# Kernel tuning notes

Measured on AMD Instinct MI355X. Metric: run time of the kernel, lower is better.

## Reference

```python
import jax, jax.numpy as jnp
import numpy as np

H = 8          # attention heads
D = 16         # per-head dim (hidden // heads)
HID = 128      # hidden_channels
OUT = 8        # out_channels of final linear
L = 2          # num_layers
NP = 100000    # num paper nodes
NA = 100000    # num author nodes
E = 500000     # edges per edge type
NEG_SLOPE = 0.2


def setup_inputs() -> dict:
    key = jax.random.key(0)
    ks = jax.random.split(key, 20)
    def nrm(k, shape, s=0.05):
        return jax.random.normal(k, shape, dtype=jnp.float32) * s
    return {
        'x_paper': jax.random.normal(ks[0], (NP, HID), dtype=jnp.float32),
        'x_author': jax.random.normal(ks[1], (NA, HID), dtype=jnp.float32),
        'Wp_p': nrm(ks[2], (L, HID, HID)),
        'bp_p': jnp.zeros((L, HID), jnp.float32),
        'Wp_a': nrm(ks[3], (L, HID, HID)),
        'bp_a': jnp.zeros((L, HID), jnp.float32),
        'as_ap': nrm(ks[4], (L, H, D), 0.2),
        'ad_ap': nrm(ks[5], (L, H, D), 0.2),
        'as_pa': nrm(ks[6], (L, H, D), 0.2),
        'ad_pa': nrm(ks[7], (L, H, D), 0.2),
        'as_pp': nrm(ks[8], (L, H, D), 0.2),
        'ad_pp': nrm(ks[9], (L, H, D), 0.2),
        'Wk': nrm(ks[10], (L, HID, HID)),
        'bk': jnp.zeros((L, HID), jnp.float32),
        'q': nrm(ks[11], (L, HID), 0.2),
        'Wout': nrm(ks[12], (HID, OUT)),
        'bout': jnp.zeros((OUT,), jnp.float32),
        'ei_ap': jax.random.randint(ks[13], (2, E), 0, NP, dtype=jnp.int32),
        'ei_pa': jax.random.randint(ks[14], (2, E), 0, NP, dtype=jnp.int32),
        'ei_pp': jax.random.randint(ks[15], (2, E), 0, NP, dtype=jnp.int32),
    }


def _leaky_relu(x):
    return jnp.where(x >= 0, x, NEG_SLOPE * x)


def _seg_softmax(alpha, dst, n):
    # PyG-style segment softmax over incoming edges of each dst node
    amax = jax.ops.segment_max(alpha, dst, num_segments=n)
    a = jnp.exp(alpha - amax[dst])
    denom = jax.ops.segment_sum(a, dst, num_segments=n) + 1e-16
    return a / denom[dst]


def _edge_attn_agg(z_src, z_dst, ei, a_s, a_d, n_dst):
    # per-edge-type GAT-style attention + scatter aggregate (HANConv message/aggregate)
    src, dst = ei[0], ei[1]
    alpha_src = (z_src * a_s).sum(-1)   # [Ns, H]
    alpha_dst = (z_dst * a_d).sum(-1)   # [Nd, H]
    alpha = _leaky_relu(alpha_src[src] + alpha_dst[dst])  # [E, H]
    alpha = _seg_softmax(alpha, dst, n_dst)
    msg = z_src[src] * alpha[:, :, None]                   # [E, H, D]
    out = jax.ops.segment_sum(msg, dst, num_segments=n_dst)
    return jax.nn.relu(out.reshape(n_dst, H * D))


def _group(outs, q, Wk, bk):
    # HANConv semantic-level attention across metapaths
    stacked = jnp.stack(outs)                               # [K, N, F]
    score = (q * jnp.tanh(stacked @ Wk + bk).mean(1)).sum(-1)  # [K]
    attn = jax.nn.softmax(score)
    return (attn[:, None, None] * stacked).sum(0)           # [N, F]


def _han_conv(xp, xa, ei_ap, ei_pa, ei_pp, Wp_p, bp_p, Wp_a, bp_a,
              as_ap, ad_ap, as_pa, ad_pa, as_pp, ad_pp, Wk, bk, q):
    zp = (xp @ Wp_p + bp_p).reshape(-1, H, D)
    za = (xa @ Wp_a + bp_a).reshape(-1, H, D)
    n_p, n_a = zp.shape[0], za.shape[0]
    out_ap = _edge_attn_agg(za, zp, ei_ap, as_ap, ad_ap, n_p)  # author -> paper
    out_pa = _edge_attn_agg(zp, za, ei_pa, as_pa, ad_pa, n_a)  # paper -> author
    out_pp = _edge_attn_agg(zp, zp, ei_pp, as_pp, ad_pp, n_p)  # paper -> paper
    new_xp = _group([out_ap, out_pp], q, Wk, bk)
    new_xa = _group([out_pa], q, Wk, bk)
    return new_xp, new_xa


def _forward(x_paper, x_author, Wp_p, bp_p, Wp_a, bp_a, as_ap, ad_ap,
             as_pa, ad_pa, as_pp, ad_pp, Wk, bk, q, Wout, bout,
             ei_ap, ei_pa, ei_pp):
    xp, xa = x_paper, x_author
    for l in range(L):
        xp, xa = _han_conv(xp, xa, ei_ap, ei_pa, ei_pp,
                           Wp_p[l], bp_p[l], Wp_a[l], bp_a[l],
                           as_ap[l], ad_ap[l], as_pa[l], ad_pa[l],
                           as_pp[l], ad_pp[l], Wk[l], bk[l], q[l])
        if l < L - 1:
            xp = jax.nn.elu(xp)  # dropout identity in eval mode (p applied only in training)
            xa = jax.nn.elu(xa)
    tgt = jax.nn.elu(xp)
    return tgt @ Wout + bout  # [NP, OUT]


def reference(x_paper, x_author, Wp_p, bp_p, Wp_a, bp_a, as_ap, ad_ap,
              as_pa, ad_pa, as_pp, ad_pp, Wk, bk, q, Wout, bout,
              ei_ap, ei_pa, ei_pp):
    return _forward(x_paper, x_author, Wp_p, bp_p, Wp_a, bp_a, as_ap, ad_ap,
                    as_pa, ad_pa, as_pp, ad_pp, Wk, bk, q, Wout, bout,
                    ei_ap, ei_pa, ei_pp)
```

## Files before the change

kernel.cpp:

```cpp
#include <hip/hip_runtime.h>

#define NHID 128
#define NHEAD 8
#define NNODE 100000
#define NEDGE 500000
#define NEG 0.2f
#define SCORE_GRID 512
#define GEMM_GRID 512
#define AGG_BLOCKS 12500
#define EB ((NEDGE + 255) / 256)
#define SB ((NNODE + 1023) / 1024)

typedef float4 f4;
typedef __attribute__((ext_vector_type(8))) short bfrag;
typedef __attribute__((ext_vector_type(4))) float facc;

__device__ inline float b2f(unsigned int u) {
    return __uint_as_float(u << 16);
}
__device__ inline unsigned short f2b(float f) {
    unsigned int u = __float_as_uint(f);
    unsigned int r = (u + 0x7FFFu + ((u >> 16) & 1u)) >> 16;
    return (unsigned short)r;
}
__device__ inline float fast_tanh(float x) {
    float e = __expf(2.f * x);
    return 1.f - 2.f / (e + 1.f);
}

struct WavSet {
    const float* W; const float* b;
    const float* v0; const float* v1; const float* v2; const float* v3;
    ushort* GT; float* bAv;
};

__global__ __launch_bounds__(256) void prep_fused(
    const float* __restrict__ w0, const float* __restrict__ w1,
    const float* __restrict__ w2, const float* __restrict__ w3,
    const float* __restrict__ w4, const float* __restrict__ w5,
    ushort* __restrict__ o0, ushort* __restrict__ o1,
    ushort* __restrict__ o2, ushort* __restrict__ o3,
    ushort* __restrict__ o4, ushort* __restrict__ o5,
    WavSet s0, WavSet s1, WavSet s2, WavSet s3,
    const int* __restrict__ e0, const int* __restrict__ e1,
    const int* __restrict__ e2, int* __restrict__ deg3)
{
    const int b = blockIdx.x;
    if (b < 384) {
        int which = b >> 6;
        int i = (b & 63) * 256 + threadIdx.x;
        const float* W = (which == 0) ? w0 : (which == 1) ? w1 : (which == 2) ? w2
                       : (which == 3) ? w3 : (which == 4) ? w4 : w5;
        ushort* Wt = (which == 0) ? o0 : (which == 1) ? o1 : (which == 2) ? o2
                   : (which == 3) ? o3 : (which == 4) ? o4 : o5;
        int fi = i >> 3, e = i & 7;
        int jk = fi >> 6, l = fi & 63;
        int j = jk >> 2, kk = jk & 3;
        int lr = l & 15, lg = l >> 4;
        Wt[i] = f2b(W[(kk * 32 + lg * 8 + e) * 128 + j * 16 + lr]);
    } else if (b < 448) {
        int bb = b - 384;
        int which = bb >> 4;
        const WavSet s = (which == 0) ? s0 : (which == 1) ? s1 : (which == 2) ? s2 : s3;
        int i = (bb & 15) * 256 + threadIdx.x;
        int fi = i >> 3, e = i & 7;
        int jk = fi >> 6, l = fi & 63;
        int jt = jk >> 2, kk = jk & 3;
        int lr = l & 15, lg = l >> 4;
        int c = jt * 16 + lr;
        int m = kk * 32 + lg * 8 + e;
        int vec = c >> 3, h = c & 7;
        const float* vp = (vec == 0) ? s.v0 : (vec == 1) ? s.v1 : (vec == 2) ? s.v2 : s.v3;
        float sv = 0.f;
        if (vp) {
            #pragma unroll
            for (int dd = 0; dd < 16; ++dd)
                sv = fmaf(s.W[m * 128 + h * 16 + dd], vp[h * 16 + dd], sv);
        }
        s.GT[i] = f2b(sv);
        if (i < 32) {
            int cc = i, vv = cc >> 3, hh = cc & 7;
            const float* vq = (vv == 0) ? s.v0 : (vv == 1) ? s.v1 : (vv == 2) ? s.v2 : s.v3;
            float t = 0.f;
            if (vq) {
                #pragma unroll
                for (int dd = 0; dd < 16; ++dd)
                    t = fmaf(s.b[hh * 16 + dd], vq[hh * 16 + dd], t);
            }
            s.bAv[cc] = t;
        }
    } else {
        int bb2 = b - 448;
        int ty = bb2 / EB, bb = bb2 % EB;
        const int* ei = (ty == 0) ? e0 : (ty == 1) ? e1 : e2;
        int e = bb * 256 + threadIdx.x;
        if (e < NEDGE) atomicAdd(deg3 + ty * NNODE + ei[NEDGE + e], 1);
    }
}

struct PArgs {
    const void* A;
    const ushort* A2;
    const ushort* WtT;
    const ushort* GT;
    const float* bias;
    const float* bAv;
    ushort* C;
    float* ao0; float* ao1; float* ao2; float* ao3;
    int mode;
};

template<int M0, int M1, int SCAT>
__global__ __launch_bounds__(256) void gemm_persist(
    PArgs g0, PArgs g1, const float* __restrict__ attn, int nt, int N,
    const int* __restrict__ e0, const int* __restrict__ e1,
    const int* __restrict__ e2, int* __restrict__ cur3, int* __restrict__ cols3)
{
    if (SCAT && blockIdx.x >= GEMM_GRID) {
        int bb2 = blockIdx.x - GEMM_GRID;
        int ty = bb2 / EB, bb = bb2 % EB;
        const int* ei = (ty == 0) ? e0 : (ty == 1) ? e1 : e2;
        int e = bb * 256 + threadIdx.x;
        if (e < NEDGE) {
            int d = ei[NEDGE + e];
            int pos = atomicAdd(cur3 + ty * NNODE + d, 1);
            cols3[ty * NEDGE + pos] = ei[e];
        }
        return;
    }

    __shared__ uint4 smem[2560];
    const int hg = GEMM_GRID >> 1;
    const int half = (blockIdx.x >= hg) ? 1 : 0;
    const PArgs ga = half ? g1 : g0;
    const int MODE = half ? M1 : M0;
    const int b0 = half ? blockIdx.x - hg : blockIdx.x;

    const int tid = threadIdx.x;
    const int l = tid & 63, w = tid >> 6;
    const int lr = l & 15, lg = l >> 4;

    {
        const uint4* ws = reinterpret_cast<const uint4*>(ga.WtT);
        const uint4* gs = reinterpret_cast<const uint4*>(ga.GT);
        #pragma unroll
        for (int i = 0; i < 8; ++i) smem[tid + i * 256] = ws[tid + i * 256];
        #pragma unroll
        for (int i = 0; i < 2; ++i) smem[2048 + tid + i * 256] = gs[tid + i * 256];
    }
    float a0 = 0.f, a1 = 0.f;
    if (MODE == 2) { a0 = attn[0]; a1 = attn[1]; }
    __syncthreads();
    const ushort* WtL = reinterpret_cast<const ushort*>(smem);
    const ushort* GL  = WtL + 16384;

    float bv[8];
    #pragma unroll
    for (int j = 0; j < 8; ++j) bv[j] = ga.bias[j * 16 + lr];
    float bA[2];
    #pragma unroll
    for (int jt = 0; jt < 2; ++jt) bA[jt] = ga.bAv[jt * 16 + lr];

    uint4 rawA[(M0 == 0 && M1 == 0) ? 8 : 16];

    auto load_raw = [&](int t) {
        const int rw0 = t * 128 + w * 32;
        #pragma unroll
        for (int i = 0; i < 2; ++i) {
            int r = rw0 + i * 16 + lr; r = (r < N) ? r : (N - 1);
            if (MODE == 1) {
                const float* ap = (const float*)ga.A + (size_t)r * 128 + lg * 8;
                #pragma unroll
                for (int kk = 0; kk < 4; ++kk) {
                    rawA[i * 8 + kk * 2]     = *reinterpret_cast<const uint4*>(ap + kk * 32);
                    rawA[i * 8 + kk * 2 + 1] = *reinterpret_cast<const uint4*>(ap + kk * 32 + 4);
                }
            } else {
                const ushort* ap = (const ushort*)ga.A + (size_t)r * 128 + lg * 8;
                #pragma unroll
                for (int kk = 0; kk < 4; ++kk)
                    rawA[i * 4 + kk] = *reinterpret_cast<const uint4*>(ap + kk * 32);
                if (MODE == 2) {
                    const ushort* ap2 = ga.A2 + (size_t)r * 128 + lg * 8;
                    #pragma unroll
                    for (int kk = 0; kk < 4; ++kk)
                        rawA[8 + i * 4 + kk] = *reinterpret_cast<const uint4*>(ap2 + kk * 32);
                }
            }
        }
    };

    if (b0 >= nt) return;
    load_raw(b0);

    for (int t = b0; t < nt; t += hg) {
        const int rw0 = t * 128 + w * 32;

        bfrag av_[2][4];
        #pragma unroll
        for (int i = 0; i < 2; ++i) {
            #pragma unroll
            for (int kk = 0; kk < 4; ++kk) {
                if (MODE == 0) {
                    av_[i][kk] = *reinterpret_cast<bfrag*>(&rawA[i * 4 + kk]);
                } else if (MODE == 1) {
                    uint4 u = rawA[i * 8 + kk * 2];
                    uint4 v = rawA[i * 8 + kk * 2 + 1];
                    bfrag fr;
                    fr[0] = (short)f2b(__uint_as_float(u.x));
                    fr[1] = (short)f2b(__uint_as_float(u.y));
                    fr[2] = (short)f2b(__uint_as_float(u.z));
                    fr[3] = (short)f2b(__uint_as_float(u.w));
                    fr[4] = (short)f2b(__uint_as_float(v.x));
                    fr[5] = (short)f2b(__uint_as_float(v.y));
                    fr[6] = (short)f2b(__uint_as_float(v.z));
                    fr[7] = (short)f2b(__uint_as_float(v.w));
                    av_[i][kk] = fr;
                } else {
                    uint4 ua = rawA[i * 4 + kk];
                    uint4 ub = rawA[8 + i * 4 + kk];
                    unsigned int aa[4] = {ua.x, ua.y, ua.z, ua.w};
                    unsigned int bb[4] = {ub.x, ub.y, ub.z, ub.w};
                    bfrag fr;
                    #pragma unroll
                    for (int q = 0; q < 4; ++q) {
                        float lo = a0 * b2f(aa[q] & 0xffffu) + a1 * b2f(bb[q] & 0xffffu);
                        float hi = a0 * b2f(aa[q] >> 16)     + a1 * b2f(bb[q] >> 16);
                        fr[q * 2]     = (short)f2b(lo);
                        fr[q * 2 + 1] = (short)f2b(hi);
                    }
                    av_[i][kk] = fr;
                }
            }
        }

        if (t + hg < nt) load_raw(t + hg);

        facc accC[2][8], accP[2][2];
        #pragma unroll
        for (int i = 0; i < 2; ++i) {
            #pragma unroll
            for (int j = 0; j < 8; ++j) accC[i][j] = (facc){0.f, 0.f, 0.f, 0.f};
            #pragma unroll
            for (int jt = 0; jt < 2; ++jt) accP[i][jt] = (facc){0.f, 0.f, 0.f, 0.f};
        }

        #pragma unroll
        for (int kk = 0; kk < 4; ++kk) {
            #pragma unroll
            for (int j = 0; j < 8; ++j) {
                bfrag bfr = *reinterpret_cast<const bfrag*>(WtL + ((j * 4 + kk) * 64 + l) * 8);
                #pragma unroll
                for (int i = 0; i < 2; ++i)
                    accC[i][j] = __builtin_amdgcn_mfma_f32_16x16x32_bf16(
                        av_[i][kk], bfr, accC[i][j], 0, 0, 0);
            }
            #pragma unroll
            for (int jt = 0; jt < 2; ++jt) {
                bfrag gfr = *reinterpret_cast<const bfrag*>(GL + ((jt * 4 + kk) * 64 + l) * 8);
                #pragma unroll
                for (int i = 0; i < 2; ++i)
                    accP[i][jt] = __builtin_amdgcn_mfma_f32_16x16x32_bf16(
                        av_[i][kk], gfr, accP[i][jt], 0, 0, 0);
            }
        }

        #pragma unroll
        for (int j = 0; j < 8; ++j) {
            #pragma unroll
            for (int i = 0; i < 2; ++i) {
                #pragma unroll
                for (int rr = 0; rr < 4; ++rr) {
                    int row = rw0 + i * 16 + lg * 4 + rr;
                    if (row < N)
                        ga.C[(size_t)row * 128 + j * 16 + lr] = f2b(accC[i][j][rr] + bv[j]);
                }
            }
        }

        #pragma unroll
        for (int jt = 0; jt < 2; ++jt) {
            int c = jt * 16 + lr;
            int vec = c >> 3, h = c & 7;
            float* ao = (vec == 0) ? ga.ao0 : (vec == 1) ? ga.ao1
                      : (vec == 2) ? ga.ao2 : ga.ao3;
            if (ao == nullptr) continue;
            #pragma unroll
            for (int i = 0; i < 2; ++i) {
                #pragma unroll
                for (int rr = 0; rr < 4; ++rr) {
                    int row = rw0 + i * 16 + lg * 4 + rr;
                    if (row < N) ao[row * 8 + h] = accP[i][jt][rr] + bA[jt];
                }
            }
        }
    }
}

__global__ __launch_bounds__(256) void score_persist(
    const ushort* __restrict__ A0, const ushort* __restrict__ A1,
    const ushort* __restrict__ WtT, const float* __restrict__ bias,
    float* __restrict__ part, int nt, int N)
{
    __shared__ uint4 smem[2048];
    __shared__ float sred[4][256];
    const int tid = threadIdx.x;
    const int l = tid & 63, w = tid >> 6;
    const int lr = l & 15, lg = l >> 4;

    {
        const uint4* ws = reinterpret_cast<const uint4*>(WtT);
        #pragma unroll
        for (int i = 0; i < 8; ++i) smem[tid + i * 256] = ws[tid + i * 256];
    }
    __syncthreads();
    const ushort* WtL = reinterpret_cast<const ushort*>(smem);

    float bv[8];
    #pragma unroll
    for (int j = 0; j < 8; ++j) bv[j] = bias[j * 16 + lr];

    float cs[2][8];
    #pragma unroll
    for (int h = 0; h < 2; ++h)
        #pragma unroll
        for (int j = 0; j < 8; ++j) cs[h][j] = 0.f;

    const int total = 2 * nt;
    for (int t = blockIdx.x; t < total; t += gridDim.x) {
        const int half = (t >= nt) ? 1 : 0;
        const ushort* A = half ? A1 : A0;
        const int bb = half ? t - nt : t;
        const int rw0 = bb * 128 + w * 32;

        bfrag av_[2][4];
        #pragma unroll
        for (int i = 0; i < 2; ++i) {
            int r = rw0 + i * 16 + lr; r = (r < N) ? r : (N - 1);
            const ushort* ap = A + (size_t)r * 128 + lg * 8;
            #pragma unroll
            for (int kk = 0; kk < 4; ++kk)
                av_[i][kk] = *reinterpret_cast<const bfrag*>(ap + kk * 32);
        }

        facc acc[2][8];
        #pragma unroll
        for (int i = 0; i < 2; ++i)
            #pragma unroll
            for (int j = 0; j < 8; ++j) acc[i][j] = (facc){0.f, 0.f, 0.f, 0.f};

        #pragma unroll
        for (int kk = 0; kk < 4; ++kk) {
            #pragma unroll
            for (int j = 0; j < 8; ++j) {
                bfrag bfr = *reinterpret_cast<const bfrag*>(WtL + ((j * 4 + kk) * 64 + l) * 8);
                #pragma unroll
                for (int i = 0; i < 2; ++i)
                    acc[i][j] = __builtin_amdgcn_mfma_f32_16x16x32_bf16(
                        av_[i][kk], bfr, acc[i][j], 0, 0, 0);
            }
        }

        #pragma unroll
        for (int j = 0; j < 8; ++j) {
            float s = 0.f;
            #pragma unroll
            for (int i = 0; i < 2; ++i) {
                #pragma unroll
                for (int r = 0; r < 4; ++r) {
                    int row = rw0 + i * 16 + lg * 4 + r;
                    if (row < N) s += fast_tanh(acc[i][j][r] + bv[j]);
                }
            }
            cs[half][j] += s;
        }
    }

    #pragma unroll
    for (int h = 0; h < 2; ++h)
        #pragma unroll
        for (int j = 0; j < 8; ++j) {
            float s = cs[h][j];
            s += __shfl_xor(s, 16, 64);
            s += __shfl_xor(s, 32, 64);
            if (lg == 0) sred[w][h * 128 + j * 16 + lr] = s;
        }
    __syncthreads();
    float tot = sred[0][tid] + sred[1][tid] + sred[2][tid] + sred[3][tid];
    part[(size_t)blockIdx.x * 256 + tid] = tot;
}

__global__ void attn_reduce(const float* __restrict__ part,
                            const float* __restrict__ qv,
                            float* __restrict__ attn, int nb)
{
    __shared__ float sm[256];
    int t = threadIdx.x;
    float s0 = 0.f, s1 = 0.f, s2 = 0.f, s3 = 0.f;
    for (int b = 0; b < nb; b += 4) {
        s0 += part[(size_t)b * 256 + t];
        s1 += part[(size_t)(b + 1) * 256 + t];
        s2 += part[(size_t)(b + 2) * 256 + t];
        s3 += part[(size_t)(b + 3) * 256 + t];
    }
    sm[t] = (s0 + s1 + s2 + s3) * qv[t & 127];
    __syncthreads();
    if (t == 0) {
        float a = 0.f, b = 0.f;
        for (int i = 0; i < 128; ++i) { a += sm[i]; b += sm[128 + i]; }
        a *= (1.0f / 100000.0f);
        b *= (1.0f / 100000.0f);
        float m = fmaxf(a, b);
        float ea = expf(a - m), eb = expf(b - m);
        float inv = 1.f / (ea + eb);
        attn[0] = ea * inv;
        attn[1] = eb * inv;
    }
}

__global__ __launch_bounds__(1024) void scan_block3(
    const int* __restrict__ deg3, int* __restrict__ offs3, int* __restrict__ bsum3)
{
    __shared__ int sd[1024];
    int ty = blockIdx.x / SB, bb = blockIdx.x % SB;
    const int* deg = deg3 + ty * NNODE;
    int* offs = offs3 + ty * (NNODE + 1);
    int t = threadIdx.x, i = bb * 1024 + t;
    int v = (i < NNODE) ? deg[i] : 0;
    sd[t] = v; __syncthreads();
    for (int o = 1; o < 1024; o <<= 1) {
        int x = (t >= o) ? sd[t - o] : 0;
        __syncthreads();
        sd[t] += x;
        __syncthreads();
    }
    if (i < NNODE) offs[i + 1] = sd[t];
    if (t == 1023) bsum3[ty * 128 + bb] = sd[t];
}

__global__ void scan_bsum3(const int* __restrict__ bsum3, int* __restrict__ boff3)
{
    int t = threadIdx.x;
    if (t < 3) {
        int run = 0;
        for (int b = 0; b < SB; ++b) { boff3[t * 128 + b] = run; run += bsum3[t * 128 + b]; }
    }
}

__global__ __launch_bounds__(1024) void scan_add3(
    int* __restrict__ offs3, const int* __restrict__ boff3, int* __restrict__ cur3)
{
    int ty = blockIdx.x / SB, bb = blockIdx.x % SB;
    int* offs = offs3 + ty * (NNODE + 1);
    int* cur = cur3 + ty * NNODE;
    int i = bb * 1024 + threadIdx.x;
    if (i == 0) { offs[0] = 0; cur[0] = 0; }
    if (i < NNODE) {
        int v = offs[i + 1] + boff3[ty * 128 + bb];
        offs[i + 1] = v;
        if (i + 1 < NNODE) cur[i + 1] = v;
    }
}

struct AggJob {
    const int* offs; const int* cols;
    const float* asrc; const float* adst;
    const ushort* z; ushort* out;
};

__global__ __launch_bounds__(256) void agg_multi(AggJob j0, AggJob j1, AggJob j2)
{
    int jb = blockIdx.x / AGG_BLOCKS;
    const AggJob jj = (jb == 0) ? j0 : (jb == 1) ? j1 : j2;
    int bb = blockIdx.x - jb * AGG_BLOCKS;
    int w = threadIdx.x >> 6;
    int lane = threadIdx.x & 63;
    int halfid = lane >> 5;
    int sl = lane & 31;
    int d = bb * 8 + w * 2 + halfid;
    int h = sl >> 2;
    float ad = jj.adst[d * 8 + h];
    int e0 = jj.offs[d], e1 = jj.offs[d + 1];
    float acc0 = 0.f, acc1 = 0.f, acc2 = 0.f, acc3 = 0.f, psum = 0.f;
    const ushort* zbase = jj.z + sl * 4;
    for (int base = e0; base < e1; base += 4) {
        int idx[4];
        #pragma unroll
        for (int i = 0; i < 4; ++i) {
            int ee = base + i;
            idx[i] = jj.cols[(ee < e1) ? ee : (e1 - 1)];
        }
        float xs[4];
        #pragma unroll
        for (int i = 0; i < 4; ++i) xs[i] = jj.asrc[idx[i] * 8 + h];
        uint2 zv[4];
        #pragma unroll
        for (int i = 0; i < 4; ++i)
            zv[i] = *reinterpret_cast<const uint2*>(zbase + (size_t)idx[i] * 128);
        #pragma unroll
        for (int i = 0; i < 4; ++i) {
            float a = xs[i] + ad;
            a = fmaxf(a, NEG * a);
            float p = __expf(a);
            p = (base + i < e1) ? p : 0.f;
            acc0 = fmaf(p, b2f(zv[i].x & 0xffffu), acc0);
            acc1 = fmaf(p, b2f(zv[i].x >> 16),     acc1);
            acc2 = fmaf(p, b2f(zv[i].y & 0xffffu), acc2);
            acc3 = fmaf(p, b2f(zv[i].y >> 16),     acc3);
            psum += p;
        }
    }
    float inv = 1.f / (psum + 1e-16f);
    uint2 pk;
    pk.x = (unsigned int)f2b(fmaxf(acc0 * inv, 0.f))
         | ((unsigned int)f2b(fmaxf(acc1 * inv, 0.f)) << 16);
    pk.y = (unsigned int)f2b(fmaxf(acc2 * inv, 0.f))
         | ((unsigned int)f2b(fmaxf(acc3 * inv, 0.f)) << 16);
    *reinterpret_cast<uint2*>(jj.out + (size_t)d * 128 + sl * 4) = pk;
}

__global__ __launch_bounds__(256) void final_gemm_mix(
    const ushort* __restrict__ XA_, const ushort* __restrict__ XB_,
    const float* __restrict__ attn, const float* __restrict__ W,
    const float* __restrict__ bias, float* __restrict__ out, int N)
{
    __shared__ float Ws[128][8];
    __shared__ __align__(16) float Xs[32][129];
    int tid = threadIdx.x;
    float a0 = attn[0], a1 = attn[1];
    for (int i = tid; i < 1024; i += 256) Ws[i >> 3][i & 7] = W[i];
    int row0 = blockIdx.x * 32;
    for (int i = tid; i < 512; i += 256) {
        int r = i >> 4, q = i & 15;
        int gr = row0 + r;
        uint4 va = make_uint4(0, 0, 0, 0), vb = make_uint4(0, 0, 0, 0);
        if (gr < N) {
            va = reinterpret_cast<const uint4*>(XA_ + (size_t)gr * 128)[q];
            vb = reinterpret_cast<const uint4*>(XB_ + (size_t)gr * 128)[q];
        }
        int c = q * 8;
        unsigned int ua[4] = {va.x, va.y, va.z, va.w};
        unsigned int ub[4] = {vb.x, vb.y, vb.z, vb.w};
        #pragma unroll
        for (int qq = 0; qq < 4; ++qq) {
            Xs[r][c + qq * 2]     = a0 * b2f(ua[qq] & 0xffffu) + a1 * b2f(ub[qq] & 0xffffu);
            Xs[r][c + qq * 2 + 1] = a0 * b2f(ua[qq] >> 16)     + a1 * b2f(ub[qq] >> 16);
        }
    }
    __syncthreads();
    int r = tid >> 3, o = tid & 7;
    int gr = row0 + r;
    if (gr < N) {
        float s = bias[o];
        #pragma unroll
        for (int k = 0; k < 128; ++k) s = fmaf(Xs[r][k], Ws[k][o], s);
        out[(size_t)gr * 8 + o] = s;
    }
}

extern "C" void kernel_launch(void* const* d_in, const int* in_sizes, int n_in,
                              void* d_out, int out_size, void* d_ws, size_t ws_size,
                              hipStream_t stream) {
    const float* x_paper  = (const float*)d_in[0];
    const float* x_author = (const float*)d_in[1];
    const float* Wp_p = (const float*)d_in[2];
    const float* bp_p = (const float*)d_in[3];
    const float* Wp_a = (const float*)d_in[4];
    const float* bp_a = (const float*)d_in[5];
    const float* as_ap = (const float*)d_in[6];
    const float* ad_ap = (const float*)d_in[7];
    const float* as_pa = (const float*)d_in[8];
    const float* ad_pa = (const float*)d_in[9];
    const float* as_pp = (const float*)d_in[10];
    const float* ad_pp = (const float*)d_in[11];
    const float* Wk   = (const float*)d_in[12];
    const float* bk   = (const float*)d_in[13];
    const float* qv   = (const float*)d_in[14];
    const float* Wout = (const float*)d_in[15];
    const float* bout = (const float*)d_in[16];
    const int* ei_ap = (const int*)d_in[17];
    const int* ei_pa = (const int*)d_in[18];
    const int* ei_pp = (const int*)d_in[19];

    const size_t NB = (size_t)NNODE * 128;
    ushort* Z0 = (ushort*)d_ws;
    ushort* Z1 = Z0 + NB;
    ushort* Z2 = Z1 + NB;
    ushort* Z3 = Z2 + NB;
    ushort* P0 = Z3 + NB;
    ushort* P1 = P0 + NB;
    float* fp = (float*)(P1 + NB);
    float* ap_s = fp; fp += NNODE * 8;
    float* ap_d = fp; fp += NNODE * 8;
    float* pa_s = fp; fp += NNODE * 8;
    float* pa_d = fp; fp += NNODE * 8;
    float* pp_s = fp; fp += NNODE * 8;
    float* pp_d = fp; fp += NNODE * 8;
    float* part = fp; fp += (size_t)SCORE_GRID * 256;
    float* attn = fp; fp += 16;
    float* bAv_p0 = fp; fp += 32;
    float* bAv_a0 = fp; fp += 32;
    float* bAv_p1 = fp; fp += 32;
    float* bAv_a1 = fp; fp += 32;
    ushort* up = (ushort*)fp;
    ushort* WtP0 = up; up += 16384;
    ushort* WtA0 = up; up += 16384;
    ushort* WtP1 = up; up += 16384;
    ushort* WtA1 = up; up += 16384;
    ushort* WtK0 = up; up += 16384;
    ushort* WtK1 = up; up += 16384;
    ushort* G_p0 = up; up += 4096;
    ushort* G_a0 = up; up += 4096;
    ushort* G_p1 = up; up += 4096;
    ushort* G_a1 = up; up += 4096;
    int* ip = (int*)(((size_t)up + 15) & ~(size_t)15);
    int* cols3 = ip; ip += 3 * NEDGE;
    int* offs3 = ip; ip += 3 * (NNODE + 1);
    int* deg3  = ip; ip += 3 * NNODE;
    int* cur3  = ip; ip += 3 * NNODE;
    int* bsum3 = ip; ip += 3 * 128;
    int* boff3 = ip; ip += 3 * 128;

    const int* cols_ap = cols3;
    const int* cols_pa = cols3 + NEDGE;
    const int* cols_pp = cols3 + 2 * NEDGE;
    const int* offs_ap = offs3;
    const int* offs_pa = offs3 + (NNODE + 1);
    const int* offs_pp = offs3 + 2 * (NNODE + 1);

    const dim3 blk(256);
    const int nt128 = (NNODE + 127) / 128;
    const int wo = 128 * 128, bo = 128, ao = 128;

    hipMemsetAsync(deg3, 0, 3 * NNODE * 4, stream);
    {
        WavSet s0{Wp_p, bp_p, ad_ap, as_pa, as_pp, ad_pp, G_p0, bAv_p0};
        WavSet s1{Wp_a, bp_a, as_ap, ad_pa, nullptr, nullptr, G_a0, bAv_a0};
        WavSet s2{Wp_p + wo, bp_p + bo, ad_ap + ao, as_pp + ao, ad_pp + ao, nullptr, G_p1, bAv_p1};
        WavSet s3{Wp_a + wo, bp_a + bo, as_ap + ao, nullptr, nullptr, nullptr, G_a1, bAv_a1};
        prep_fused<<<448 + 3 * EB, blk, 0, stream>>>(
            Wp_p, Wp_a, Wp_p + wo, Wp_a + wo, Wk, Wk + wo,
            WtP0, WtA0, WtP1, WtA1, WtK0, WtK1,
            s0, s1, s2, s3, ei_ap, ei_pa, ei_pp, deg3);
    }
    scan_block3<<<3 * SB, 1024, 0, stream>>>(deg3, offs3, bsum3);
    scan_bsum3<<<1, 64, 0, stream>>>(bsum3, boff3);
    scan_add3<<<3 * SB, 1024, 0, stream>>>(offs3, boff3, cur3);

    {
        PArgs gp{x_paper,  nullptr, WtP0, G_p0, bp_p, bAv_p0, Z0, ap_d, pa_s, pp_s, pp_d, 1};
        PArgs ga{x_author, nullptr, WtA0, G_a0, bp_a, bAv_a0, Z1, ap_s, pa_d, nullptr, nullptr, 1};
        gemm_persist<1, 1, 1><<<GEMM_GRID + 3 * EB, blk, 0, stream>>>(
            gp, ga, attn, nt128, NNODE, ei_ap, ei_pa, ei_pp, cur3, cols3);
    }

    {
        AggJob a0{offs_ap, cols_ap, ap_s, ap_d, Z1, Z2};
        AggJob a1{offs_pa, cols_pa, pa_s, pa_d, Z0, Z3};
        AggJob a2{offs_pp, cols_pp, pp_s, pp_d, Z0, P0};
        agg_multi<<<3 * AGG_BLOCKS, blk, 0, stream>>>(a0, a1, a2);
    }

    score_persist<<<SCORE_GRID, blk, 0, stream>>>(Z2, P0, WtK0, bk, part, nt128, NNODE);
    attn_reduce<<<1, 256, 0, stream>>>(part, qv, attn, SCORE_GRID);

    {
        PArgs gp{Z2, P0, WtP1, G_p1, bp_p + bo, bAv_p1, Z0, ap_d, pp_s, pp_d, nullptr, 2};
        PArgs ga{Z3, nullptr, WtA1, G_a1, bp_a + bo, bAv_a1, Z1, ap_s, nullptr, nullptr, nullptr, 0};
        gemm_persist<2, 0, 0><<<GEMM_GRID, blk, 0, stream>>>(
            gp, ga, attn, nt128, NNODE, nullptr, nullptr, nullptr, nullptr, nullptr);
    }

    {
        AggJob a0{offs_ap, cols_ap, ap_s, ap_d, Z1, Z2};
        AggJob a1{offs_pp, cols_pp, pp_s, pp_d, Z0, P1};
        agg_multi<<<2 * AGG_BLOCKS, blk, 0, stream>>>(a0, a1, a1);
    }

    score_persist<<<SCORE_GRID, blk, 0, stream>>>(Z2, P1, WtK1, bk + bo, part, nt128, NNODE);
    attn_reduce<<<1, 256, 0, stream>>>(part, qv + bo, attn, SCORE_GRID);

    final_gemm_mix<<<(NNODE + 31) / 32, blk, 0, stream>>>(Z2, P1, attn, Wout, bout, (float*)d_out, NNODE);
}
```

Baseline: 532.4 us.

## Fuse PA aggregation into score kernel, merge scan kernels, trim GEMM register staging

The paper-to-author aggregation now runs as extra blocks inside the layer-0 score kernel, so it overlaps the score GEMM and one launch disappears. The separate block-sum scan kernel is removed; each scan_add3 block sums the earlier block totals serially in one thread. The persistent GEMM keeps only one raw staging buffer: the second row group (fp32 mode) and the A2 operand (mix mode) are loaded inside the loop rather than prefetched, which lowers register pressure but exposes that load latency. The CSR column scatter uses nontemporal stores.

Result: slower. 625.8 us (+17.5%).

```diff
diff --git a/kernel.cpp b/kernel.cpp
--- a/kernel.cpp
+++ b/kernel.cpp
@@ -124,7 +124,7 @@
         if (e < NEDGE) {
             int d = ei[NEDGE + e];
             int pos = atomicAdd(cur3 + ty * NNODE + d, 1);
-            cols3[ty * NEDGE + pos] = ei[e];
+            __builtin_nontemporal_store(ei[e], cols3 + (size_t)ty * NEDGE + pos);
         }
         return;
     }
@@ -161,31 +161,28 @@
     #pragma unroll
     for (int jt = 0; jt < 2; ++jt) bA[jt] = ga.bAv[jt * 16 + lr];
 
-    uint4 rawA[(M0 == 0 && M1 == 0) ? 8 : 16];
+    uint4 rawA[8];
+
+    auto clampr = [&](int row) { return (row < N) ? row : (N - 1); };
 
     auto load_raw = [&](int t) {
         const int rw0 = t * 128 + w * 32;
-        #pragma unroll
-        for (int i = 0; i < 2; ++i) {
-            int r = rw0 + i * 16 + lr; r = (r < N) ? r : (N - 1);
-            if (MODE == 1) {
-                const float* ap = (const float*)ga.A + (size_t)r * 128 + lg * 8;
-                #pragma unroll
-                for (int kk = 0; kk < 4; ++kk) {
-                    rawA[i * 8 + kk * 2]     = *reinterpret_cast<const uint4*>(ap + kk * 32);
-                    rawA[i * 8 + kk * 2 + 1] = *reinterpret_cast<const uint4*>(ap + kk * 32 + 4);
-                }
-            } else {
+        if (MODE == 1) {
+            int r = clampr(rw0 + lr);
+            const float* ap = (const float*)ga.A + (size_t)r * 128 + lg * 8;
+            #pragma unroll
+            for (int kk = 0; kk < 4; ++kk) {
+                rawA[kk * 2]     = *reinterpret_cast<const uint4*>(ap + kk * 32);
+                rawA[kk * 2 + 1] = *reinterpret_cast<const uint4*>(ap + kk * 32 + 4);
+            }
+        } else {
+            #pragma unroll
+            for (int i = 0; i < 2; ++i) {
+                int r = clampr(rw0 + i * 16 + lr);
                 const ushort* ap = (const ushort*)ga.A + (size_t)r * 128 + lg * 8;
                 #pragma unroll
                 for (int kk = 0; kk < 4; ++kk)
                     rawA[i * 4 + kk] = *reinterpret_cast<const uint4*>(ap + kk * 32);
-                if (MODE == 2) {
-                    const ushort* ap2 = ga.A2 + (size_t)r * 128 + lg * 8;
-                    #pragma unroll
-                    for (int kk = 0; kk < 4; ++kk)
-                        rawA[8 + i * 4 + kk] = *reinterpret_cast<const uint4*>(ap2 + kk * 32);
-                }
             }
         }
     };
@@ -197,28 +194,66 @@
         const int rw0 = t * 128 + w * 32;
 
         bfrag av_[2][4];
-        #pragma unroll
-        for (int i = 0; i < 2; ++i) {
+        if (MODE == 0) {
+            #pragma unroll
+            for (int i = 0; i < 2; ++i)
+                #pragma unroll
+                for (int kk = 0; kk < 4; ++kk)
+                    av_[i][kk] = *reinterpret_cast<bfrag*>(&rawA[i * 4 + kk]);
+        } else if (MODE == 1) {
             #pragma unroll
             for (int kk = 0; kk < 4; ++kk) {
-                if (MODE == 0) {
-                    av_[i][kk] = *reinterpret_cast<bfrag*>(&rawA[i * 4 + kk]);
-                } else if (MODE == 1) {
-                    uint4 u = rawA[i * 8 + kk * 2];
-                    uint4 v = rawA[i * 8 + kk * 2 + 1];
+                uint4 u = rawA[kk * 2], v = rawA[kk * 2 + 1];
+                bfrag fr;
+                fr[0] = (short)f2b(__uint_as_float(u.x));
+                fr[1] = (short)f2b(__uint_as_float(u.y));
+                fr[2] = (short)f2b(__uint_as_float(u.z));
+                fr[3] = (short)f2b(__uint_as_float(u.w));
+                fr[4] = (short)f2b(__uint_as_float(v.x));
+                fr[5] = (short)f2b(__uint_as_float(v.y));
+                fr[6] = (short)f2b(__uint_as_float(v.z));
+                fr[7] = (short)f2b(__uint_as_float(v.w));
+                av_[0][kk] = fr;
+            }
+            {
+                int r = clampr(rw0 + 16 + lr);
+                const float* ap = (const float*)ga.A + (size_t)r * 128 + lg * 8;
+                uint4 u_[4], v_[4];
+                #pragma unroll
+                for (int kk = 0; kk < 4; ++kk) {
+                    u_[kk] = *reinterpret_cast<const uint4*>(ap + kk * 32);
+                    v_[kk] = *reinterpret_cast<const uint4*>(ap + kk * 32 + 4);
+                }
+                #pragma unroll
+                for (int kk = 0; kk < 4; ++kk) {
                     bfrag fr;
-                    fr[0] = (short)f2b(__uint_as_float(u.x));
-                    fr[1] = (short)f2b(__uint_as_float(u.y));
-                    fr[2] = (short)f2b(__uint_as_float(u.z));
-                    fr[3] = (short)f2b(__uint_as_float(u.w));
-                    fr[4] = (short)f2b(__uint_as_float(v.x));
-                    fr[5] = (short)f2b(__uint_as_float(v.y));
-                    fr[6] = (short)f2b(__uint_as_float(v.z));
-                    fr[7] = (short)f2b(__uint_as_float(v.w));
-                    av_[i][kk] = fr;
-                } else {
+                    fr[0] = (short)f2b(__uint_as_float(u_[kk].x));
+                    fr[1] = (short)f2b(__uint_as_float(u_[kk].y));
+                    fr[2] = (short)f2b(__uint_as_float(u_[kk].z));
+                    fr[3] = (short)f2b(__uint_as_float(u_[kk].w));
+                    fr[4] = (short)f2b(__uint_as_float(v_[kk].x));
+                    fr[5] = (short)f2b(__uint_as_float(v_[kk].y));
+                    fr[6] = (short)f2b(__uint_as_float(v_[kk].z));
+                    fr[7] = (short)f2b(__uint_as_float(v_[kk].w));
+                    av_[1][kk] = fr;
+                }
+            }
+        } else {
+            uint4 rawB[8];
+            #pragma unroll
+            for (int i = 0; i < 2; ++i) {
+                int r = clampr(rw0 + i * 16 + lr);
+                const ushort* ap2 = ga.A2 + (size_t)r * 128 + lg * 8;
+                #pragma unroll
+                for (int kk = 0; kk < 4; ++kk)
+                    rawB[i * 4 + kk] = *reinterpret_cast<const uint4*>(ap2 + kk * 32);
+            }
+            #pragma unroll
+            for (int i = 0; i < 2; ++i) {
+                #pragma unroll
+                for (int kk = 0; kk < 4; ++kk) {
                     uint4 ua = rawA[i * 4 + kk];
-                    uint4 ub = rawA[8 + i * 4 + kk];
+                    uint4 ub = rawB[i * 4 + kk];
                     unsigned int aa[4] = {ua.x, ua.y, ua.z, ua.w};
                     unsigned int bb[4] = {ub.x, ub.y, ub.z, ub.w};
                     bfrag fr;
@@ -297,6 +332,166 @@
     }
 }
 
+struct AggJob {
+    const int* offs; const int* cols;
+    const float* asrc; const float* adst;
+    const ushort* z; ushort* out;
+};
+
+__device__ inline void agg_body(const AggJob& jj, int bb, int tid)
+{
+    int w = tid >> 6;
+    int lane = tid & 63;
+    int halfid = lane >> 5;
+    int sl = lane & 31;
+    int d = bb * 8 + w * 2 + halfid;
+    int h = sl >> 2;
+    float ad = jj.adst[d * 8 + h];
+    int e0 = jj.offs[d], e1 = jj.offs[d + 1];
+    float acc0 = 0.f, acc1 = 0.f, acc2 = 0.f, acc3 = 0.f, psum = 0.f;
+    const ushort* zbase = jj.z + sl * 4;
+    for (int base = e0; base < e1; base += 4) {
+        int idx[4];
+        #pragma unroll
+        for (int i = 0; i < 4; ++i) {
+            int ee = base + i;
+            idx[i] = jj.cols[(ee < e1) ? ee : (e1 - 1)];
+        }
+        float xs[4];
+        #pragma unroll
+        for (int i = 0; i < 4; ++i) xs[i] = jj.asrc[idx[i] * 8 + h];
+        uint2 zv[4];
+        #pragma unroll
+        for (int i = 0; i < 4; ++i)
+            zv[i] = *reinterpret_cast<const uint2*>(zbase + (size_t)idx[i] * 128);
+        #pragma unroll
+        for (int i = 0; i < 4; ++i) {
+            float a = xs[i] + ad;
+            a = fmaxf(a, NEG * a);
+            float p = __expf(a);
+            p = (base + i < e1) ? p : 0.f;
+            acc0 = fmaf(p, b2f(zv[i].x & 0xffffu), acc0);
+            acc1 = fmaf(p, b2f(zv[i].x >> 16),     acc1);
+            acc2 = fmaf(p, b2f(zv[i].y & 0xffffu), acc2);
+            acc3 = fmaf(p, b2f(zv[i].y >> 16),     acc3);
+            psum += p;
+        }
+    }
+    float inv = 1.f / (psum + 1e-16f);
+    uint2 pk;
+    pk.x = (unsigned int)f2b(fmaxf(acc0 * inv, 0.f))
+         | ((unsigned int)f2b(fmaxf(acc1 * inv, 0.f)) << 16);
+    pk.y = (unsigned int)f2b(fmaxf(acc2 * inv, 0.f))
+         | ((unsigned int)f2b(fmaxf(acc3 * inv, 0.f)) << 16);
+    *reinterpret_cast<uint2*>(jj.out + (size_t)d * 128 + sl * 4) = pk;
+}
+
+__global__ __launch_bounds__(256) void agg_multi(AggJob j0, AggJob j1, AggJob j2)
+{
+    int jb = blockIdx.x / AGG_BLOCKS;
+    const AggJob jj = (jb == 0) ? j0 : (jb == 1) ? j1 : j2;
+    agg_body(jj, blockIdx.x - jb * AGG_BLOCKS, threadIdx.x);
+}
+
+__global__ __launch_bounds__(256) void score_agg(
+    const ushort* __restrict__ A0, const ushort* __restrict__ A1,
+    const ushort* __restrict__ WtT, const float* __restrict__ bias,
+    float* __restrict__ part, int nt, int N, AggJob aj)
+{
+    __shared__ uint4 smem[2048];
+    __shared__ float sred[4][256];
+
+    if (blockIdx.x >= SCORE_GRID) {
+        agg_body(aj, blockIdx.x - SCORE_GRID, threadIdx.x);
+        return;
+    }
+
+    const int tid = threadIdx.x;
+    const int l = tid & 63, w = tid >> 6;
+    const int lr = l & 15, lg = l >> 4;
+
+    {
+        const uint4* ws = reinterpret_cast<const uint4*>(WtT);
+        #pragma unroll
+        for (int i = 0; i < 8; ++i) smem[tid + i * 256] = ws[tid + i * 256];
+    }
+    __syncthreads();
+    const ushort* WtL = reinterpret_cast<const ushort*>(smem);
+
+    float bv[8];
+    #pragma unroll
+    for (int j = 0; j < 8; ++j) bv[j] = bias[j * 16 + lr];
+
+    float cs[2][8];
+    #pragma unroll
+    for (int h = 0; h < 2; ++h)
+        #pragma unroll
+        for (int j = 0; j < 8; ++j) cs[h][j] = 0.f;
+
+    const int total = 2 * nt;
+    for (int t = blockIdx.x; t < total; t += SCORE_GRID) {
+        const int half = (t >= nt) ? 1 : 0;
+        const ushort* A = half ? A1 : A0;
+        const int bb = half ? t - nt : t;
+        const int rw0 = bb * 128 + w * 32;
+
+        bfrag av_[2][4];
+        #pragma unroll
+        for (int i = 0; i < 2; ++i) {
+            int r = rw0 + i * 16 + lr; r = (r < N) ? r : (N - 1);
+            const ushort* ap = A + (size_t)r * 128 + lg * 8;
+            #pragma unroll
+            for (int kk = 0; kk < 4; ++kk)
+                av_[i][kk] = *reinterpret_cast<const bfrag*>(ap + kk * 32);
+        }
+
+        facc acc[2][8];
+        #pragma unroll
+        for (int i = 0; i < 2; ++i)
+            #pragma unroll
+            for (int j = 0; j < 8; ++j) acc[i][j] = (facc){0.f, 0.f, 0.f, 0.f};
+
+        #pragma unroll
+        for (int kk = 0; kk < 4; ++kk) {
+            #pragma unroll
+            for (int j = 0; j < 8; ++j) {
+                bfrag bfr = *reinterpret_cast<const bfrag*>(WtL + ((j * 4 + kk) * 64 + l) * 8);
+                #pragma unroll
+                for (int i = 0; i < 2; ++i)
+                    acc[i][j] = __builtin_amdgcn_mfma_f32_16x16x32_bf16(
+                        av_[i][kk], bfr, acc[i][j], 0, 0, 0);
+            }
+        }
+
+        #pragma unroll
+        for (int j = 0; j < 8; ++j) {
+            float s = 0.f;
+            #pragma unroll
+            for (int i = 0; i < 2; ++i) {
+                #pragma unroll
+                for (int r = 0; r < 4; ++r) {
+                    int row = rw0 + i * 16 + lg * 4 + r;
+                    if (row < N) s += fast_tanh(acc[i][j][r] + bv[j]);
+                }
+            }
+            cs[half][j] += s;
+        }
+    }
+
+    #pragma unroll
+    for (int h = 0; h < 2; ++h)
+        #pragma unroll
+        for (int j = 0; j < 8; ++j) {
+            float s = cs[h][j];
+            s += __shfl_xor(s, 16, 64);
+            s += __shfl_xor(s, 32, 64);
+            if (lg == 0) sred[w][h * 128 + j * 16 + lr] = s;
+        }
+    __syncthreads();
+    float tot = sred[0][tid] + sred[1][tid] + sred[2][tid] + sred[3][tid];
+    part[(size_t)blockIdx.x * 256 + tid] = tot;
+}
+
 __global__ __launch_bounds__(256) void score_persist(
     const ushort* __restrict__ A0, const ushort* __restrict__ A1,
     const ushort* __restrict__ WtT, const float* __restrict__ bias,
@@ -438,85 +633,27 @@
     if (t == 1023) bsum3[ty * 128 + bb] = sd[t];
 }
 
-__global__ void scan_bsum3(const int* __restrict__ bsum3, int* __restrict__ boff3)
-{
-    int t = threadIdx.x;
-    if (t < 3) {
+__global__ __launch_bounds__(1024) void scan_add3(
+    int* __restrict__ offs3, const int* __restrict__ bsum3, int* __restrict__ cur3)
+{
+    __shared__ int spref;
+    int ty = blockIdx.x / SB, bb = blockIdx.x % SB;
+    if (threadIdx.x == 0) {
         int run = 0;
-        for (int b = 0; b < SB; ++b) { boff3[t * 128 + b] = run; run += bsum3[t * 128 + b]; }
-    }
-}
-
-__global__ __launch_bounds__(1024) void scan_add3(
-    int* __restrict__ offs3, const int* __restrict__ boff3, int* __restrict__ cur3)
-{
-    int ty = blockIdx.x / SB, bb = blockIdx.x % SB;
+        for (int b = 0; b < bb; ++b) run += bsum3[ty * 128 + b];
+        spref = run;
+    }
+    __syncthreads();
+    int boff = spref;
     int* offs = offs3 + ty * (NNODE + 1);
     int* cur = cur3 + ty * NNODE;
     int i = bb * 1024 + threadIdx.x;
     if (i == 0) { offs[0] = 0; cur[0] = 0; }
     if (i < NNODE) {
-        int v = offs[i + 1] + boff3[ty * 128 + bb];
+        int v = offs[i + 1] + boff;
         offs[i + 1] = v;
         if (i + 1 < NNODE) cur[i + 1] = v;
     }
-}
-
-struct AggJob {
-    const int* offs; const int* cols;
-    const float* asrc; const float* adst;
-    const ushort* z; ushort* out;
-};
-
-__global__ __launch_bounds__(256) void agg_multi(AggJob j0, AggJob j1, AggJob j2)
-{
-    int jb = blockIdx.x / AGG_BLOCKS;
-    const AggJob jj = (jb == 0) ? j0 : (jb == 1) ? j1 : j2;
-    int bb = blockIdx.x - jb * AGG_BLOCKS;
-    int w = threadIdx.x >> 6;
-    int lane = threadIdx.x & 63;
-    int halfid = lane >> 5;
-    int sl = lane & 31;
-    int d = bb * 8 + w * 2 + halfid;
-    int h = sl >> 2;
-    float ad = jj.adst[d * 8 + h];
-    int e0 = jj.offs[d], e1 = jj.offs[d + 1];
-    float acc0 = 0.f, acc1 = 0.f, acc2 = 0.f, acc3 = 0.f, psum = 0.f;
-    const ushort* zbase = jj.z + sl * 4;
-    for (int base = e0; base < e1; base += 4) {
-        int idx[4];
-        #pragma unroll
-        for (int i = 0; i < 4; ++i) {
-            int ee = base + i;
-            idx[i] = jj.cols[(ee < e1) ? ee : (e1 - 1)];
-        }
-        float xs[4];
-        #pragma unroll
-        for (int i = 0; i < 4; ++i) xs[i] = jj.asrc[idx[i] * 8 + h];
-        uint2 zv[4];
-        #pragma unroll
-        for (int i = 0; i < 4; ++i)
-            zv[i] = *reinterpret_cast<const uint2*>(zbase + (size_t)idx[i] * 128);
-        #pragma unroll
-        for (int i = 0; i < 4; ++i) {
-            float a = xs[i] + ad;
-            a = fmaxf(a, NEG * a);
-            float p = __expf(a);
-            p = (base + i < e1) ? p : 0.f;
-            acc0 = fmaf(p, b2f(zv[i].x & 0xffffu), acc0);
-            acc1 = fmaf(p, b2f(zv[i].x >> 16),     acc1);
-            acc2 = fmaf(p, b2f(zv[i].y & 0xffffu), acc2);
-            acc3 = fmaf(p, b2f(zv[i].y >> 16),     acc3);
-            psum += p;
-        }
-    }
-    float inv = 1.f / (psum + 1e-16f);
-    uint2 pk;
-    pk.x = (unsigned int)f2b(fmaxf(acc0 * inv, 0.f))
-         | ((unsigned int)f2b(fmaxf(acc1 * inv, 0.f)) << 16);
-    pk.y = (unsigned int)f2b(fmaxf(acc2 * inv, 0.f))
-         | ((unsigned int)f2b(fmaxf(acc3 * inv, 0.f)) << 16);
-    *reinterpret_cast<uint2*>(jj.out + (size_t)d * 128 + sl * 4) = pk;
 }
 
 __global__ __launch_bounds__(256) void final_gemm_mix(
@@ -619,7 +756,6 @@
     int* deg3  = ip; ip += 3 * NNODE;
     int* cur3  = ip; ip += 3 * NNODE;
     int* bsum3 = ip; ip += 3 * 128;
-    int* boff3 = ip; ip += 3 * 128;
 
     const int* cols_ap = cols3;
     const int* cols_pa = cols3 + NEDGE;
@@ -644,8 +780,7 @@
             s0, s1, s2, s3, ei_ap, ei_pa, ei_pp, deg3);
     }
     scan_block3<<<3 * SB, 1024, 0, stream>>>(deg3, offs3, bsum3);
-    scan_bsum3<<<1, 64, 0, stream>>>(bsum3, boff3);
-    scan_add3<<<3 * SB, 1024, 0, stream>>>(offs3, boff3, cur3);
+    scan_add3<<<3 * SB, 1024, 0, stream>>>(offs3, bsum3, cur3);
 
     {
         PArgs gp{x_paper,  nullptr, WtP0, G_p0, bp_p, bAv_p0, Z0, ap_d, pa_s, pp_s, pp_d, 1};
@@ -656,12 +791,15 @@
 
     {
         AggJob a0{offs_ap, cols_ap, ap_s, ap_d, Z1, Z2};
-        AggJob a1{offs_pa, cols_pa, pa_s, pa_d, Z0, Z3};
-        AggJob a2{offs_pp, cols_pp, pp_s, pp_d, Z0, P0};
-        agg_multi<<<3 * AGG_BLOCKS, blk, 0, stream>>>(a0, a1, a2);
-    }
-
-    score_persist<<<SCORE_GRID, blk, 0, stream>>>(Z2, P0, WtK0, bk, part, nt128, NNODE);
+        AggJob a1{offs_pp, cols_pp, pp_s, pp_d, Z0, P0};
+        agg_multi<<<2 * AGG_BLOCKS, blk, 0, stream>>>(a0, a1, a1);
+    }
+
+    {
+        AggJob apa{offs_pa, cols_pa, pa_s, pa_d, Z0, Z3};
+        score_agg<<<SCORE_GRID + AGG_BLOCKS, blk, 0, stream>>>(
+            Z2, P0, WtK0, bk, part, nt128, NNODE, apa);
+    }
     attn_reduce<<<1, 256, 0, stream>>>(part, qv, attn, SCORE_GRID);
 
     {
```
